# Performance work log

Hardware: AMD Instinct MI355X
Metric: run time of the kernel (lower is better)

## Reference

```python
import jax, jax.numpy as jnp
import numpy as np

N_KERNELS = 11

def _kernel_mus(n):
    l = [1.0]
    bs = 2.0 / (n - 1)
    l.append(1 - bs / 2)
    for i in range(1, n - 1):
        l.append(l[i] - bs)
    return l

def _kernel_sigmas(n):
    bs = 2.0 / (n - 1)
    return [0.001] + [0.5 * bs] * (n - 1)

MU = jnp.asarray(_kernel_mus(N_KERNELS), jnp.float32)      # [K]
SIGMA = jnp.asarray(_kernel_sigmas(N_KERNELS), jnp.float32)  # [K]


def setup_inputs() -> dict:
    key = jax.random.key(0)
    ks = jax.random.split(key, 10)
    V, E, C = 50000, 300, 128
    B, Q, D = 128, 30, 200
    inp = {
        'query_tokens': jax.random.randint(ks[0], (B, Q), 0, V),
        'document_tokens': jax.random.randint(ks[1], (B, D), 0, V),
        'embedding': jax.random.normal(ks[2], (V, E), jnp.float32) * 0.1,
        'conv_w1': jax.random.normal(ks[3], (C, E, 1), jnp.float32) * 0.05,
        'conv_w2': jax.random.normal(ks[4], (C, E, 2), jnp.float32) * 0.05,
        'conv_w3': jax.random.normal(ks[5], (C, E, 3), jnp.float32) * 0.05,
        'conv_b1': jax.random.normal(ks[6], (C,), jnp.float32) * 0.01,
        'conv_b2': jax.random.normal(ks[7], (C,), jnp.float32) * 0.01,
        'conv_b3': jax.random.normal(ks[8], (C,), jnp.float32) * 0.01,
        'dense_w': jax.random.uniform(ks[9], (1, N_KERNELS * 9), jnp.float32, -0.014, 0.014),
    }
    return inp


def _conv_ngram(x_ble, w, b):
    # x_ble: [B, L, E]; w: [C, E, k]; pad (0, k-1) on the length dim -> same length out
    x = x_ble.transpose(0, 2, 1)  # [B, E, L]
    y = jax.lax.conv_general_dilated(
        x, w, window_strides=(1,), padding=[(0, w.shape[2] - 1)],
        dimension_numbers=('NCH', 'OIH', 'NCH'))
    return jax.nn.relu(y + b[None, :, None]).transpose(0, 2, 1)  # [B, L, C]


def _kernel_pool(q, d, qd_mask, q_mask):
    # q: [B,Q,C], d: [B,D,C]; cosine sim -> Gaussian RBF soft-binning -> masked log-sum pooling
    qn = q / (jnp.linalg.norm(q, axis=-1, keepdims=True) + 1e-13)
    dn = d / (jnp.linalg.norm(d, axis=-1, keepdims=True) + 1e-13)
    cos = jnp.einsum('bqc,bdc->bqd', qn, dn) * qd_mask           # [B,Q,D]
    diff = cos[..., None] - MU                                    # [B,Q,D,K]
    kern = jnp.exp(-(diff * diff) / (2.0 * SIGMA * SIGMA)) * qd_mask[..., None]
    per_kernel_query = jnp.sum(kern, axis=2)                      # [B,Q,K]
    logk = jnp.log(jnp.clip(per_kernel_query, 1e-10)) * 0.01
    return jnp.sum(logk * q_mask[..., None], axis=1)              # [B,K]


def reference(query_tokens, document_tokens, embedding,
              conv_w1, conv_w2, conv_w3, conv_b1, conv_b2, conv_b3, dense_w):
    q_mask = (query_tokens > 0).astype(jnp.float32)               # [B,Q]
    d_mask = (document_tokens > 0).astype(jnp.float32)            # [B,D]
    qd_mask = q_mask[:, :, None] * d_mask[:, None, :]             # [B,Q,D]

    q_emb = embedding[query_tokens]                               # [B,Q,E]
    d_emb = embedding[document_tokens]                            # [B,D,E]

    convs = [(conv_w1, conv_b1), (conv_w2, conv_b2), (conv_w3, conv_b3)]
    q_grams = [_conv_ngram(q_emb, w, b) for w, b in convs]
    d_grams = [_conv_ngram(d_emb, w, b) for w, b in convs]

    feats = jnp.concatenate(
        [_kernel_pool(q, d, qd_mask, q_mask) for q in q_grams for d in d_grams],
        axis=1)                                                   # [B, K*9]
    return (feats @ dense_w.T)[:, 0]                              # [B]
```

## Files before the change

### kernel.cpp

```cpp
#include <hip/hip_runtime.h>
#include <hip/hip_bf16.h>
#include <math.h>

#define B_   128
#define Qn   30
#define Dn   200
#define En   300

typedef __attribute__((ext_vector_type(8))) short short8;
typedef __attribute__((ext_vector_type(4))) float floatx4;
typedef unsigned int u32;
typedef unsigned short u16;

typedef const __attribute__((address_space(1))) unsigned int* gas_ptr;
typedef __attribute__((address_space(3))) unsigned int* las_ptr;

static __device__ __forceinline__ void gld_lds16(const void* g, void* l) {
    __builtin_amdgcn_global_load_lds((gas_ptr)g, (las_ptr)l, 16, 0, 0);
}

static __device__ __forceinline__ u16 f2b(float x) {
    union { float f; u32 u; } v; v.f = x;
    u32 r = v.u + 0x7FFFu + ((v.u >> 16) & 1u);
    return (u16)(r >> 16);
}
static __device__ __forceinline__ float bits2f(u32 u) {
    union { u32 u2; float f; } v; v.u2 = u; return v.f;
}

__global__ void prep_gather_kernel(
    const int* __restrict__ qtok, const int* __restrict__ dtok,
    const float* __restrict__ emb,
    const float* __restrict__ w1, const float* __restrict__ w2, const float* __restrict__ w3,
    u16* __restrict__ Ag, u16* __restrict__ Wt2)
{
    const int tid = threadIdx.x;
    if (blockIdx.x < 16) {
        const int b = blockIdx.y, c = blockIdx.x;
        __shared__ int toks[16];
        if (tid < 16) {
            int pos = c*16 + tid;
            int tok = -1;
            if (pos < Dn) tok = dtok[b*Dn + pos];
            else if (pos >= 208 && pos < 238) tok = qtok[b*Qn + (pos - 208)];
            toks[tid] = tok;
        }
        __syncthreads();
        #pragma unroll
        for (int i = 0; i < 5; ++i) {
            int f = tid + i*256;
            int r = f / 80, c4 = f - r*80;
            int t = toks[r];
            u16 o0=0,o1=0,o2=0,o3=0;
            if (t >= 0 && c4 < 75) {
                float4 v = *(const float4*)(emb + t*En + c4*4);
                o0=f2b(v.x); o1=f2b(v.y); o2=f2b(v.z); o3=f2b(v.w);
            }
            u16* p = Ag + ((b*256 + c*16 + r)*320 + c4*4);
            p[0]=o0; p[1]=o1; p[2]=o2; p[3]=o3;
        }
        if (b == 127 && c == 15 && tid < 160) {
            u16* p = Ag + (32768*320) + tid*4;
            p[0]=0; p[1]=0; p[2]=0; p[3]=0;
        }
    } else {
        int p = ((blockIdx.x - 16)*128 + blockIdx.y)*256 + tid;
        if (p >= 245760) return;
        int g, ntap, o;
        if (p < 40960)       { g=0; ntap=1; o=p; }
        else if (p < 122880) { g=1; ntap=2; o=p-40960; }
        else                 { g=2; ntap=3; o=p-122880; }
        int ks = o / (ntap*4096);
        int r  = o - ks*(ntap*4096);
        int j  = r / 4096;
        int r2 = r & 4095;
        int nt = r2 >> 9;
        int r3 = r2 & 511;
        int q4 = r3 >> 7;
        int c16 = (r3 >> 3) & 15;
        int k8 = r3 & 7;
        int ch = nt*16 + c16;
        int e  = ks*32 + q4*8 + k8;
        float v = 0.f;
        if (e < En) {
            if (g == 0)      v = w1[ch*En + e];
            else if (g == 1) v = w2[(ch*En + e)*2 + j];
            else             v = w3[(ch*En + e)*3 + j];
        }
        Wt2[p] = f2b(v);
    }
}

template<int NTAP>
static __device__ __forceinline__ void conv_body(
    const u16* __restrict__ Ag, const u16* __restrict__ Wt2g,
    const float* __restrict__ bp,
    u16* __restrict__ qg, u16* __restrict__ dg,
    float* __restrict__ invnq, float* __restrict__ invnd,
    int gram, char* smem)
{
    char* As = smem;
    char* Bs = smem + 43296;

    const int tid = threadIdx.x;
    const int tile = blockIdx.x;
    const int wv = tid >> 6, lane = tid & 63;
    const int l15 = lane & 15, qd4 = lane >> 4;
    const int mh = wv >> 1, nh = wv & 1;

    {
        const char* src = (const char*)Wt2g + lane*16;
        #pragma unroll
        for (int i = 0; i < NTAP*2; ++i) {
            int chunk = wv*NTAP*2 + i;
            gld_lds16(src + chunk*1024, Bs + chunk*1024);
        }
    }
    {
        const char* base = (const char*)Ag + (size_t)tile*64*640;
        #pragma unroll
        for (int i = 0; i < 11; ++i) {
            int idx = tid + i*256;
            if (idx < 2640) {
                int r = idx / 40, c = idx - r*40;
                uint4 v = *(const uint4*)(base + r*640 + c*16);
                *(uint4*)(As + r*656 + c*16) = v;
            }
        }
    }

    float bias[4];
    #pragma unroll
    for (int nt = 0; nt < 4; ++nt) bias[nt] = bp[nh*64 + nt*16 + l15];

    floatx4 acc[2][4];
    #pragma unroll
    for (int mt = 0; mt < 2; ++mt)
        #pragma unroll
        for (int nt = 0; nt < 4; ++nt)
            acc[mt][nt] = (floatx4){0.f,0.f,0.f,0.f};

    __syncthreads();

    short8 af[2][NTAP];
    #pragma unroll
    for (int mt = 0; mt < 2; ++mt)
        #pragma unroll
        for (int j = 0; j < NTAP; ++j)
            af[mt][j] = *(const short8*)(As + (mh*32 + mt*16 + l15 + j)*656 + qd4*16);

    for (int ks = 0; ks < 10; ++ks) {
        #pragma unroll
        for (int j = 0; j < NTAP; ++j) {
            short8 bfj[4];
            #pragma unroll
            for (int nt = 0; nt < 4; ++nt)
                bfj[nt] = *(const short8*)(Bs + (j*8 + nh*4 + nt)*1024 + lane*16);
            #pragma unroll
            for (int mt = 0; mt < 2; ++mt)
                #pragma unroll
                for (int nt = 0; nt < 4; ++nt)
                    acc[mt][nt] = __builtin_amdgcn_mfma_f32_16x16x32_bf16(
                        af[mt][j], bfj[nt], acc[mt][nt], 0, 0, 0);
        }
        if (ks < 9) {
            __syncthreads();
            const char* src = (const char*)Wt2g + (ks+1)*NTAP*8192 + lane*16;
            #pragma unroll
            for (int i = 0; i < NTAP*2; ++i) {
                int chunk = wv*NTAP*2 + i;
                gld_lds16(src + chunk*1024, Bs + chunk*1024);
            }
            #pragma unroll
            for (int mt = 0; mt < 2; ++mt)
                #pragma unroll
                for (int j = 0; j < NTAP; ++j)
                    af[mt][j] = *(const short8*)(As + (mh*32 + mt*16 + l15 + j)*656 + (ks+1)*64 + qd4*16);
            __syncthreads();
        }
    }
    __syncthreads();

    u16* Gs = (u16*)Bs;
    #pragma unroll
    for (int mt = 0; mt < 2; ++mt)
        #pragma unroll
        for (int nt = 0; nt < 4; ++nt) {
            int ch = nh*64 + nt*16 + l15;
            #pragma unroll
            for (int i = 0; i < 4; ++i) {
                int row = mh*32 + mt*16 + qd4*4 + i;
                Gs[row*136 + ch] = f2b(fmaxf(acc[mt][nt][i] + bias[nt], 0.f));
            }
        }
    __syncthreads();

    if (tid < 64) {
        const char* rp = (const char*)Gs + tid*272;
        float ssum = 0.f;
        #pragma unroll
        for (int t16 = 0; t16 < 16; ++t16) {
            uint4 u = *(const uint4*)(rp + t16*16);
            float x;
            x = bits2f(u.x << 16); ssum += x*x;  x = bits2f(u.x & 0xffff0000u); ssum += x*x;
            x = bits2f(u.y << 16); ssum += x*x;  x = bits2f(u.y & 0xffff0000u); ssum += x*x;
            x = bits2f(u.z << 16); ssum += x*x;  x = bits2f(u.z & 0xffff0000u); ssum += x*x;
            x = bits2f(u.w << 16); ssum += x*x;  x = bits2f(u.w & 0xffff0000u); ssum += x*x;
        }
        float inv = 1.f / (sqrtf(ssum) + 1e-13f);
        int gR = tile*64 + tid;
        int b = gR >> 8, pos = gR & 255;
        if (pos < 208)                     invnd[(gram*B_ + b)*208 + pos] = inv;
        else if (pos < 240)                invnq[(gram*B_ + b)*32 + (pos - 208)] = inv;
    }
    #pragma unroll
    for (int i = 0; i < 4; ++i) {
        int idx = tid + i*256;
        int r = idx >> 4, c16 = idx & 15;
        uint4 v = *(const uint4*)((const char*)Gs + r*272 + c16*16);
        int gR = tile*64 + r;
        int b = gR >> 8, pos = gR & 255;
        if (pos < 208)      *(uint4*)(dg + ((gram*B_ + b)*208 + pos)*128 + c16*8) = v;
        else if (pos < 240) *(uint4*)(qg + ((gram*B_ + b)*32 + (pos - 208))*128 + c16*8) = v;
    }
}

__global__ __launch_bounds__(256, 2) void conv_kernel(
    const u16* __restrict__ Ag, const u16* __restrict__ Wt2,
    const float* __restrict__ b1, const float* __restrict__ b2, const float* __restrict__ b3,
    u16* __restrict__ qg, u16* __restrict__ dg,
    float* __restrict__ invnq, float* __restrict__ invnd)
{
    extern __shared__ char smem[];
    if (blockIdx.y == 0)
        conv_body<1>(Ag, Wt2,                       b1, qg, dg, invnq, invnd, 0, smem);
    else if (blockIdx.y == 1)
        conv_body<2>(Ag, Wt2 + 40960,               b2, qg, dg, invnq, invnd, 1, smem);
    else
        conv_body<3>(Ag, Wt2 + 122880,              b3, qg, dg, invnq, invnd, 2, smem);
}

__global__ __launch_bounds__(256, 2) void pool_kernel(
    const u16* __restrict__ qg, const u16* __restrict__ dg,
    const float* __restrict__ invnq, const float* __restrict__ invnd,
    const int* __restrict__ qtok, const int* __restrict__ dtok,
    float* __restrict__ feats)
{
    __shared__ __align__(16) u16 dsb[208*136];
    __shared__ float pk[32*12];
    __shared__ float invq[32];
    __shared__ float qm[32];
    __shared__ __align__(16) float invd[208];

    const int tid = threadIdx.x;
    const int b = blockIdx.y, combo = blockIdx.x;
    const int qi = combo / 3, dj = combo - 3*qi;
    const int wv = tid >> 6, lane = tid & 63;
    const int l15 = lane & 15, qd4 = lane >> 4;

    for (int idx = tid; idx < 208*16; idx += 256) {
        int r = idx >> 4, ch = idx & 15;
        uint4 v = make_uint4(0u,0u,0u,0u);
        if (r < Dn) v = *(const uint4*)(dg + ((dj*B_ + b)*208 + r)*128 + ch*8);
        *(uint4*)((char*)dsb + r*272 + ch*16) = v;
    }
    if (tid < 208) {
        float v = invnd[(dj*B_ + b)*208 + tid];
        bool ok = (tid < Dn) && (dtok[b*Dn + tid] > 0);
        invd[tid] = ok ? v : (-fabsf(v) - 1.0f);
    }
    if (tid < 32) {
        float v = invnq[(qi*B_ + b)*32 + tid];
        bool ok = (tid < Qn) && (qtok[b*Qn + tid] > 0);
        invq[tid] = ok ? v : 0.f;
        qm[tid] = ok ? 1.f : 0.f;
    }
    for (int i = tid; i < 384; i += 256) pk[i] = 0.f;
    __syncthreads();

    short8 qf[2][4];
    float vq[2];
    #pragma unroll
    for (int qt = 0; qt < 2; ++qt) {
        vq[qt] = invq[qt*16 + l15];
        #pragma unroll
        for (int ks = 0; ks < 4; ++ks)
            qf[qt][ks] = *(const short8*)(qg + ((qi*B_ + b)*32 + qt*16 + l15)*128 + ks*32 + qd4*8);
    }
    float pkl[2][11];
    #pragma unroll
    for (int qt = 0; qt < 2; ++qt)
        #pragma unroll
        for (int k = 0; k < 11; ++k) pkl[qt][k] = 0.f;

    const float CkR[9] = {8886110.5f, 162754.79f, 2980.958f, 54.598150f, 1.0f,
                          0.018315639f, 3.3546263e-4f, 6.1442124e-6f, 1.1253517e-7f};

    for (int t = wv; t < 13; t += 4) {
        short8 af[4];
        #pragma unroll
        for (int ks = 0; ks < 4; ++ks)
            af[ks] = *(const short8*)((const char*)dsb + (t*16 + l15)*272 + ks*64 + qd4*16);
        floatx4 acc[2];
        acc[0] = (floatx4){0.f,0.f,0.f,0.f};
        acc[1] = (floatx4){0.f,0.f,0.f,0.f};
        #pragma unroll
        for (int ks = 0; ks < 4; ++ks)
            #pragma unroll
            for (int qt = 0; qt < 2; ++qt)
                acc[qt] = __builtin_amdgcn_mfma_f32_16x16x32_bf16(af[ks], qf[qt][ks], acc[qt], 0, 0, 0);
        floatx4 iv4 = *(const floatx4*)(invd + t*16 + qd4*4);
        #pragma unroll
        for (int qt = 0; qt < 2; ++qt)
            #pragma unroll
            for (int i = 0; i < 4; ++i) {
                float cs = acc[qt][i] * vq[qt] * iv4[i];
                cs = (cs > 0.f) ? cs : 2.0f;
                float t0 = cs - 1.0f;
                float u  = cs - 0.9f;
                float s0 = __expf(-500000.f * t0 * t0);
                float e  = __expf(-50.f * u * u);
                float rr = __expf(-20.f * cs);
                pkl[qt][0] += s0;
                pkl[qt][1] += e;
                #pragma unroll
                for (int kk = 0; kk < 9; ++kk) {
                    e = e * rr * CkR[kk];
                    pkl[qt][2 + kk] += e;
                }
            }
    }
    #pragma unroll
    for (int qt = 0; qt < 2; ++qt)
        #pragma unroll
        for (int k = 0; k < 11; ++k) {
            float v = pkl[qt][k];
            v += __shfl_xor(v, 16);
            v += __shfl_xor(v, 32);
            if (qd4 == 0) atomicAdd(&pk[(qt*16 + l15)*12 + k], v);
        }
    __syncthreads();

    if (tid < 11) {
        float s = 0.f;
        for (int q = 0; q < Qn; ++q)
            s += qm[q] * 0.01f * __logf(fmaxf(pk[q*12 + tid], 1e-10f));
        feats[(b*9 + combo)*11 + tid] = s;
    }
}

__global__ void final_kernel(const float* __restrict__ feats,
                             const float* __restrict__ dw,
                             float* __restrict__ out) {
    int b = threadIdx.x;
    if (b < B_) {
        float s = 0.f;
        for (int f = 0; f < 99; ++f) s += feats[b*99 + f] * dw[f];
        out[b] = s;
    }
}

extern "C" void kernel_launch(void* const* d_in, const int* in_sizes, int n_in,
                              void* d_out, int out_size, void* d_ws, size_t ws_size,
                              hipStream_t stream) {
    const int*   qtok = (const int*)d_in[0];
    const int*   dtok = (const int*)d_in[1];
    const float* emb  = (const float*)d_in[2];
    const float* w1   = (const float*)d_in[3];
    const float* w2   = (const float*)d_in[4];
    const float* w3   = (const float*)d_in[5];
    const float* b1   = (const float*)d_in[6];
    const float* b2   = (const float*)d_in[7];
    const float* b3   = (const float*)d_in[8];
    const float* dw   = (const float*)d_in[9];
    float* out = (float*)d_out;

    char* w = (char*)d_ws;
    u16*   Wt2   = (u16*)w;
    u16*   Ag    = (u16*)(w + 491520);
    u16*   qg    = (u16*)(w + 21464320);
    u16*   dgm   = (u16*)(w + 24610048);
    float* invq_ = (float*)(w + 45057280);
    float* invd_ = (float*)(w + 45106432);
    float* feats = (float*)(w + 45425920);

    prep_gather_kernel<<<dim3(24, B_), 256, 0, stream>>>(
        qtok, dtok, emb, w1, w2, w3, Ag, Wt2);

    const int conv_lds = 43296 + 24576;
    hipFuncSetAttribute(reinterpret_cast<const void*>(conv_kernel),
                        hipFuncAttributeMaxDynamicSharedMemorySize, conv_lds);
    conv_kernel<<<dim3(512, 3), 256, conv_lds, stream>>>(
        Ag, Wt2, b1, b2, b3, qg, dgm, invq_, invd_);

    pool_kernel<<<dim3(9, B_), 256, 0, stream>>>(qg, dgm, invq_, invd_, qtok, dtok, feats);

    final_kernel<<<1, 128, 0, stream>>>(feats, dw, out);
}
```

Before: 194.5 us.

## Fuse embedding gather into conv, double-buffer weights, split trigram tiles, share doc tiles in pool

```diff
diff --git a/kernel.cpp b/kernel.cpp
--- a/kernel.cpp
+++ b/kernel.cpp
@@ -28,105 +28,87 @@
     union { u32 u2; float f; } v; v.u2 = u; return v.f;
 }
 
-__global__ void prep_gather_kernel(
+__global__ void prep_w_kernel(const float* __restrict__ w1, const float* __restrict__ w2,
+                              const float* __restrict__ w3, u16* __restrict__ Wt2) {
+    int p = blockIdx.x * 256 + threadIdx.x;
+    if (p >= 245760) return;
+    int g, ntap, o;
+    if (p < 40960)       { g=0; ntap=1; o=p; }
+    else if (p < 122880) { g=1; ntap=2; o=p-40960; }
+    else                 { g=2; ntap=3; o=p-122880; }
+    int ks = o / (ntap*4096);
+    int r  = o - ks*(ntap*4096);
+    int j  = r / 4096;
+    int r2 = r & 4095;
+    int nt = r2 >> 9;
+    int r3 = r2 & 511;
+    int q4 = r3 >> 7;
+    int c16 = (r3 >> 3) & 15;
+    int k8 = r3 & 7;
+    int ch = nt*16 + c16;
+    int e  = ks*32 + q4*8 + k8;
+    float v = 0.f;
+    if (e < En) {
+        if (g == 0)      v = w1[ch*En + e];
+        else if (g == 1) v = w2[(ch*En + e)*2 + j];
+        else             v = w3[(ch*En + e)*3 + j];
+    }
+    Wt2[p] = f2b(v);
+}
+
+template<int NTAP>
+static __device__ __forceinline__ void conv_body64(
+    int tile, int gram,
     const int* __restrict__ qtok, const int* __restrict__ dtok,
-    const float* __restrict__ emb,
-    const float* __restrict__ w1, const float* __restrict__ w2, const float* __restrict__ w3,
-    u16* __restrict__ Ag, u16* __restrict__ Wt2)
-{
-    const int tid = threadIdx.x;
-    if (blockIdx.x < 16) {
-        const int b = blockIdx.y, c = blockIdx.x;
-        __shared__ int toks[16];
-        if (tid < 16) {
-            int pos = c*16 + tid;
-            int tok = -1;
-            if (pos < Dn) tok = dtok[b*Dn + pos];
-            else if (pos >= 208 && pos < 238) tok = qtok[b*Qn + (pos - 208)];
-            toks[tid] = tok;
-        }
-        __syncthreads();
-        #pragma unroll
-        for (int i = 0; i < 5; ++i) {
-            int f = tid + i*256;
-            int r = f / 80, c4 = f - r*80;
-            int t = toks[r];
-            u16 o0=0,o1=0,o2=0,o3=0;
-            if (t >= 0 && c4 < 75) {
-                float4 v = *(const float4*)(emb + t*En + c4*4);
-                o0=f2b(v.x); o1=f2b(v.y); o2=f2b(v.z); o3=f2b(v.w);
-            }
-            u16* p = Ag + ((b*256 + c*16 + r)*320 + c4*4);
-            p[0]=o0; p[1]=o1; p[2]=o2; p[3]=o3;
-        }
-        if (b == 127 && c == 15 && tid < 160) {
-            u16* p = Ag + (32768*320) + tid*4;
-            p[0]=0; p[1]=0; p[2]=0; p[3]=0;
-        }
-    } else {
-        int p = ((blockIdx.x - 16)*128 + blockIdx.y)*256 + tid;
-        if (p >= 245760) return;
-        int g, ntap, o;
-        if (p < 40960)       { g=0; ntap=1; o=p; }
-        else if (p < 122880) { g=1; ntap=2; o=p-40960; }
-        else                 { g=2; ntap=3; o=p-122880; }
-        int ks = o / (ntap*4096);
-        int r  = o - ks*(ntap*4096);
-        int j  = r / 4096;
-        int r2 = r & 4095;
-        int nt = r2 >> 9;
-        int r3 = r2 & 511;
-        int q4 = r3 >> 7;
-        int c16 = (r3 >> 3) & 15;
-        int k8 = r3 & 7;
-        int ch = nt*16 + c16;
-        int e  = ks*32 + q4*8 + k8;
-        float v = 0.f;
-        if (e < En) {
-            if (g == 0)      v = w1[ch*En + e];
-            else if (g == 1) v = w2[(ch*En + e)*2 + j];
-            else             v = w3[(ch*En + e)*3 + j];
-        }
-        Wt2[p] = f2b(v);
-    }
-}
-
-template<int NTAP>
-static __device__ __forceinline__ void conv_body(
-    const u16* __restrict__ Ag, const u16* __restrict__ Wt2g,
+    const float* __restrict__ emb, const u16* __restrict__ Wt2g,
     const float* __restrict__ bp,
     u16* __restrict__ qg, u16* __restrict__ dg,
-    float* __restrict__ invnq, float* __restrict__ invnd,
-    int gram, char* smem)
+    float* __restrict__ invnq, float* __restrict__ invnd, char* smem)
 {
-    char* As = smem;
-    char* Bs = smem + 43296;
+    char* As  = smem;
+    char* Bs0 = smem + 43296;
+    char* Bs1 = smem + 43296 + NTAP*8192;
+    __shared__ int toks[66];
 
     const int tid = threadIdx.x;
-    const int tile = blockIdx.x;
     const int wv = tid >> 6, lane = tid & 63;
     const int l15 = lane & 15, qd4 = lane >> 4;
     const int mh = wv >> 1, nh = wv & 1;
 
+    if (tid < 66) {
+        int gR = tile*64 + tid;
+        int tok = -1;
+        if (gR < 32768) {
+            int bb = gR >> 8, pos = gR & 255;
+            if (pos < Dn) tok = dtok[bb*Dn + pos];
+            else if (pos >= 208 && pos < 238) tok = qtok[bb*Qn + (pos - 208)];
+        }
+        toks[tid] = tok;
+    }
+    __syncthreads();
+
     {
         const char* src = (const char*)Wt2g + lane*16;
         #pragma unroll
         for (int i = 0; i < NTAP*2; ++i) {
             int chunk = wv*NTAP*2 + i;
-            gld_lds16(src + chunk*1024, Bs + chunk*1024);
-        }
-    }
-    {
-        const char* base = (const char*)Ag + (size_t)tile*64*640;
-        #pragma unroll
-        for (int i = 0; i < 11; ++i) {
-            int idx = tid + i*256;
-            if (idx < 2640) {
-                int r = idx / 40, c = idx - r*40;
-                uint4 v = *(const uint4*)(base + r*640 + c*16);
-                *(uint4*)(As + r*656 + c*16) = v;
-            }
-        }
+            gld_lds16(src + chunk*1024, Bs0 + chunk*1024);
+        }
+    }
+    for (int f = tid; f < 66*75; f += 256) {
+        int row = f / 75, e4 = f - row*75;
+        int t = toks[row];
+        u16 o0=0,o1=0,o2=0,o3=0;
+        if (t >= 0) {
+            float4 v = *(const float4*)(emb + t*En + e4*4);
+            o0=f2b(v.x); o1=f2b(v.y); o2=f2b(v.z); o3=f2b(v.w);
+        }
+        u16* pp = (u16*)(As + row*656 + e4*8);
+        pp[0]=o0; pp[1]=o1; pp[2]=o2; pp[3]=o3;
+    }
+    for (int f = tid; f < 66*14; f += 256) {
+        int row = f / 14, cc = f - row*14;
+        *(u32*)(As + row*656 + 600 + cc*4) = 0u;
     }
 
     float bias[4];
@@ -142,20 +124,29 @@
 
     __syncthreads();
 
-    short8 af[2][NTAP];
-    #pragma unroll
-    for (int mt = 0; mt < 2; ++mt)
-        #pragma unroll
-        for (int j = 0; j < NTAP; ++j)
-            af[mt][j] = *(const short8*)(As + (mh*32 + mt*16 + l15 + j)*656 + qd4*16);
-
     for (int ks = 0; ks < 10; ++ks) {
+        char* Bcur = (ks & 1) ? Bs1 : Bs0;
+        char* Bnxt = (ks & 1) ? Bs0 : Bs1;
+        if (ks < 9) {
+            const char* src = (const char*)Wt2g + (ks+1)*NTAP*8192 + lane*16;
+            #pragma unroll
+            for (int i = 0; i < NTAP*2; ++i) {
+                int chunk = wv*NTAP*2 + i;
+                gld_lds16(src + chunk*1024, Bnxt + chunk*1024);
+            }
+        }
+        short8 af[2][NTAP];
+        #pragma unroll
+        for (int mt = 0; mt < 2; ++mt)
+            #pragma unroll
+            for (int j = 0; j < NTAP; ++j)
+                af[mt][j] = *(const short8*)(As + (mh*32 + mt*16 + l15 + j)*656 + ks*64 + qd4*16);
         #pragma unroll
         for (int j = 0; j < NTAP; ++j) {
             short8 bfj[4];
             #pragma unroll
             for (int nt = 0; nt < 4; ++nt)
-                bfj[nt] = *(const short8*)(Bs + (j*8 + nh*4 + nt)*1024 + lane*16);
+                bfj[nt] = *(const short8*)(Bcur + (j*8 + nh*4 + nt)*1024 + lane*16);
             #pragma unroll
             for (int mt = 0; mt < 2; ++mt)
                 #pragma unroll
@@ -163,25 +154,10 @@
                     acc[mt][nt] = __builtin_amdgcn_mfma_f32_16x16x32_bf16(
                         af[mt][j], bfj[nt], acc[mt][nt], 0, 0, 0);
         }
-        if (ks < 9) {
-            __syncthreads();
-            const char* src = (const char*)Wt2g + (ks+1)*NTAP*8192 + lane*16;
-            #pragma unroll
-            for (int i = 0; i < NTAP*2; ++i) {
-                int chunk = wv*NTAP*2 + i;
-                gld_lds16(src + chunk*1024, Bs + chunk*1024);
-            }
-            #pragma unroll
-            for (int mt = 0; mt < 2; ++mt)
-                #pragma unroll
-                for (int j = 0; j < NTAP; ++j)
-                    af[mt][j] = *(const short8*)(As + (mh*32 + mt*16 + l15 + j)*656 + (ks+1)*64 + qd4*16);
-            __syncthreads();
-        }
-    }
-    __syncthreads();
-
-    u16* Gs = (u16*)Bs;
+        __syncthreads();
+    }
+
+    u16* Gs = (u16*)As;
     #pragma unroll
     for (int mt = 0; mt < 2; ++mt)
         #pragma unroll
@@ -210,8 +186,8 @@
         float inv = 1.f / (sqrtf(ssum) + 1e-13f);
         int gR = tile*64 + tid;
         int b = gR >> 8, pos = gR & 255;
-        if (pos < 208)                     invnd[(gram*B_ + b)*208 + pos] = inv;
-        else if (pos < 240)                invnq[(gram*B_ + b)*32 + (pos - 208)] = inv;
+        if (pos < 208)      invnd[(gram*B_ + b)*208 + pos] = inv;
+        else if (pos < 238) invnq[(gram*B_ + b)*32 + (pos - 208)] = inv;
     }
     #pragma unroll
     for (int i = 0; i < 4; ++i) {
@@ -221,23 +197,168 @@
         int gR = tile*64 + r;
         int b = gR >> 8, pos = gR & 255;
         if (pos < 208)      *(uint4*)(dg + ((gram*B_ + b)*208 + pos)*128 + c16*8) = v;
-        else if (pos < 240) *(uint4*)(qg + ((gram*B_ + b)*32 + (pos - 208))*128 + c16*8) = v;
+        else if (pos < 238) *(uint4*)(qg + ((gram*B_ + b)*32 + (pos - 208))*128 + c16*8) = v;
+    }
+}
+
+static __device__ __forceinline__ void conv_body32(
+    int tile,
+    const int* __restrict__ qtok, const int* __restrict__ dtok,
+    const float* __restrict__ emb, const u16* __restrict__ Wt2g,
+    const float* __restrict__ bp,
+    u16* __restrict__ qg, u16* __restrict__ dg,
+    float* __restrict__ invnq, float* __restrict__ invnd, char* smem)
+{
+    char* As  = smem;
+    char* Bs0 = smem + 22304;
+    char* Bs1 = smem + 46880;
+    __shared__ int toks[34];
+
+    const int tid = threadIdx.x;
+    const int wv = tid >> 6, lane = tid & 63;
+    const int l15 = lane & 15, qd4 = lane >> 4;
+
+    if (tid < 34) {
+        int gR = tile*32 + tid;
+        int tok = -1;
+        if (gR < 32768) {
+            int bb = gR >> 8, pos = gR & 255;
+            if (pos < Dn) tok = dtok[bb*Dn + pos];
+            else if (pos >= 208 && pos < 238) tok = qtok[bb*Qn + (pos - 208)];
+        }
+        toks[tid] = tok;
+    }
+    __syncthreads();
+
+    {
+        const char* src = (const char*)Wt2g + lane*16;
+        #pragma unroll
+        for (int i = 0; i < 6; ++i) {
+            int chunk = wv*6 + i;
+            gld_lds16(src + chunk*1024, Bs0 + chunk*1024);
+        }
+    }
+    for (int f = tid; f < 34*75; f += 256) {
+        int row = f / 75, e4 = f - row*75;
+        int t = toks[row];
+        u16 o0=0,o1=0,o2=0,o3=0;
+        if (t >= 0) {
+            float4 v = *(const float4*)(emb + t*En + e4*4);
+            o0=f2b(v.x); o1=f2b(v.y); o2=f2b(v.z); o3=f2b(v.w);
+        }
+        u16* pp = (u16*)(As + row*656 + e4*8);
+        pp[0]=o0; pp[1]=o1; pp[2]=o2; pp[3]=o3;
+    }
+    for (int f = tid; f < 34*14; f += 256) {
+        int row = f / 14, cc = f - row*14;
+        *(u32*)(As + row*656 + 600 + cc*4) = 0u;
+    }
+
+    float bias[2];
+    #pragma unroll
+    for (int nt = 0; nt < 2; ++nt) bias[nt] = bp[wv*32 + nt*16 + l15];
+
+    floatx4 acc[2][2];
+    #pragma unroll
+    for (int mt = 0; mt < 2; ++mt)
+        #pragma unroll
+        for (int nt = 0; nt < 2; ++nt)
+            acc[mt][nt] = (floatx4){0.f,0.f,0.f,0.f};
+
+    __syncthreads();
+
+    for (int ks = 0; ks < 10; ++ks) {
+        char* Bcur = (ks & 1) ? Bs1 : Bs0;
+        char* Bnxt = (ks & 1) ? Bs0 : Bs1;
+        if (ks < 9) {
+            const char* src = (const char*)Wt2g + (ks+1)*24576 + lane*16;
+            #pragma unroll
+            for (int i = 0; i < 6; ++i) {
+                int chunk = wv*6 + i;
+                gld_lds16(src + chunk*1024, Bnxt + chunk*1024);
+            }
+        }
+        short8 af[2][3];
+        #pragma unroll
+        for (int mt = 0; mt < 2; ++mt)
+            #pragma unroll
+            for (int j = 0; j < 3; ++j)
+                af[mt][j] = *(const short8*)(As + (mt*16 + l15 + j)*656 + ks*64 + qd4*16);
+        #pragma unroll
+        for (int j = 0; j < 3; ++j) {
+            short8 bfj[2];
+            #pragma unroll
+            for (int nt = 0; nt < 2; ++nt)
+                bfj[nt] = *(const short8*)(Bcur + (j*8 + wv*2 + nt)*1024 + lane*16);
+            #pragma unroll
+            for (int mt = 0; mt < 2; ++mt)
+                #pragma unroll
+                for (int nt = 0; nt < 2; ++nt)
+                    acc[mt][nt] = __builtin_amdgcn_mfma_f32_16x16x32_bf16(
+                        af[mt][j], bfj[nt], acc[mt][nt], 0, 0, 0);
+        }
+        __syncthreads();
+    }
+
+    u16* Gs = (u16*)As;
+    #pragma unroll
+    for (int mt = 0; mt < 2; ++mt)
+        #pragma unroll
+        for (int nt = 0; nt < 2; ++nt) {
+            int ch = wv*32 + nt*16 + l15;
+            #pragma unroll
+            for (int i = 0; i < 4; ++i) {
+                int row = mt*16 + qd4*4 + i;
+                Gs[row*136 + ch] = f2b(fmaxf(acc[mt][nt][i] + bias[nt], 0.f));
+            }
+        }
+    __syncthreads();
+
+    if (tid < 32) {
+        const char* rp = (const char*)Gs + tid*272;
+        float ssum = 0.f;
+        #pragma unroll
+        for (int t16 = 0; t16 < 16; ++t16) {
+            uint4 u = *(const uint4*)(rp + t16*16);
+            float x;
+            x = bits2f(u.x << 16); ssum += x*x;  x = bits2f(u.x & 0xffff0000u); ssum += x*x;
+            x = bits2f(u.y << 16); ssum += x*x;  x = bits2f(u.y & 0xffff0000u); ssum += x*x;
+            x = bits2f(u.z << 16); ssum += x*x;  x = bits2f(u.z & 0xffff0000u); ssum += x*x;
+            x = bits2f(u.w << 16); ssum += x*x;  x = bits2f(u.w & 0xffff0000u); ssum += x*x;
+        }
+        float inv = 1.f / (sqrtf(ssum) + 1e-13f);
+        int gR = tile*32 + tid;
+        int b = gR >> 8, pos = gR & 255;
+        if (pos < 208)      invnd[(2*B_ + b)*208 + pos] = inv;
+        else if (pos < 238) invnq[(2*B_ + b)*32 + (pos - 208)] = inv;
+    }
+    #pragma unroll
+    for (int i = 0; i < 2; ++i) {
+        int idx = tid + i*256;
+        int r = idx >> 4, c16 = idx & 15;
+        uint4 v = *(const uint4*)((const char*)Gs + r*272 + c16*16);
+        int gR = tile*32 + r;
+        int b = gR >> 8, pos = gR & 255;
+        if (pos < 208)      *(uint4*)(dg + ((2*B_ + b)*208 + pos)*128 + c16*8) = v;
+        else if (pos < 238) *(uint4*)(qg + ((2*B_ + b)*32 + (pos - 208))*128 + c16*8) = v;
     }
 }
 
 __global__ __launch_bounds__(256, 2) void conv_kernel(
-    const u16* __restrict__ Ag, const u16* __restrict__ Wt2,
+    const int* __restrict__ qtok, const int* __restrict__ dtok,
+    const float* __restrict__ emb, const u16* __restrict__ Wt2,
     const float* __restrict__ b1, const float* __restrict__ b2, const float* __restrict__ b3,
     u16* __restrict__ qg, u16* __restrict__ dg,
     float* __restrict__ invnq, float* __restrict__ invnd)
 {
     extern __shared__ char smem[];
-    if (blockIdx.y == 0)
-        conv_body<1>(Ag, Wt2,                       b1, qg, dg, invnq, invnd, 0, smem);
-    else if (blockIdx.y == 1)
-        conv_body<2>(Ag, Wt2 + 40960,               b2, qg, dg, invnq, invnd, 1, smem);
+    int bx = blockIdx.x;
+    if (bx < 512)
+        conv_body64<1>(bx, 0, qtok, dtok, emb, Wt2,          b1, qg, dg, invnq, invnd, smem);
+    else if (bx < 1024)
+        conv_body64<2>(bx-512, 1, qtok, dtok, emb, Wt2+40960, b2, qg, dg, invnq, invnd, smem);
     else
-        conv_body<3>(Ag, Wt2 + 122880,              b3, qg, dg, invnq, invnd, 2, smem);
+        conv_body32(bx-1024, qtok, dtok, emb, Wt2+122880,     b3, qg, dg, invnq, invnd, smem);
 }
 
 __global__ __launch_bounds__(256, 2) void pool_kernel(
@@ -247,14 +368,13 @@
     float* __restrict__ feats)
 {
     __shared__ __align__(16) u16 dsb[208*136];
-    __shared__ float pk[32*12];
-    __shared__ float invq[32];
-    __shared__ float qm[32];
+    __shared__ float pk[96*12];
+    __shared__ float invqA[96];
+    __shared__ float qmA[96];
     __shared__ __align__(16) float invd[208];
 
     const int tid = threadIdx.x;
-    const int b = blockIdx.y, combo = blockIdx.x;
-    const int qi = combo / 3, dj = combo - 3*qi;
+    const int b = blockIdx.y, dj = blockIdx.x;
     const int wv = tid >> 6, lane = tid & 63;
     const int l15 = lane & 15, qd4 = lane >> 4;
 
@@ -269,83 +389,87 @@
         bool ok = (tid < Dn) && (dtok[b*Dn + tid] > 0);
         invd[tid] = ok ? v : (-fabsf(v) - 1.0f);
     }
-    if (tid < 32) {
-        float v = invnq[(qi*B_ + b)*32 + tid];
-        bool ok = (tid < Qn) && (qtok[b*Qn + tid] > 0);
-        invq[tid] = ok ? v : 0.f;
-        qm[tid] = ok ? 1.f : 0.f;
-    }
-    for (int i = tid; i < 384; i += 256) pk[i] = 0.f;
-    __syncthreads();
-
-    short8 qf[2][4];
-    float vq[2];
-    #pragma unroll
-    for (int qt = 0; qt < 2; ++qt) {
-        vq[qt] = invq[qt*16 + l15];
-        #pragma unroll
-        for (int ks = 0; ks < 4; ++ks)
-            qf[qt][ks] = *(const short8*)(qg + ((qi*B_ + b)*32 + qt*16 + l15)*128 + ks*32 + qd4*8);
-    }
-    float pkl[2][11];
-    #pragma unroll
-    for (int qt = 0; qt < 2; ++qt)
-        #pragma unroll
-        for (int k = 0; k < 11; ++k) pkl[qt][k] = 0.f;
+    if (tid < 96) {
+        int qi = tid >> 5, qr = tid & 31;
+        float v = invnq[(qi*B_ + b)*32 + qr];
+        bool ok = (qr < Qn) && (qtok[b*Qn + qr] > 0);
+        invqA[tid] = ok ? v : 0.f;
+        qmA[tid] = ok ? 1.f : 0.f;
+    }
+    for (int i = tid; i < 96*12; i += 256) pk[i] = 0.f;
+    __syncthreads();
 
     const float CkR[9] = {8886110.5f, 162754.79f, 2980.958f, 54.598150f, 1.0f,
                           0.018315639f, 3.3546263e-4f, 6.1442124e-6f, 1.1253517e-7f};
 
-    for (int t = wv; t < 13; t += 4) {
-        short8 af[4];
-        #pragma unroll
-        for (int ks = 0; ks < 4; ++ks)
-            af[ks] = *(const short8*)((const char*)dsb + (t*16 + l15)*272 + ks*64 + qd4*16);
-        floatx4 acc[2];
-        acc[0] = (floatx4){0.f,0.f,0.f,0.f};
-        acc[1] = (floatx4){0.f,0.f,0.f,0.f};
-        #pragma unroll
-        for (int ks = 0; ks < 4; ++ks)
+    for (int qi = 0; qi < 3; ++qi) {
+        short8 qf[2][4];
+        float vq[2];
+        #pragma unroll
+        for (int qt = 0; qt < 2; ++qt) {
+            vq[qt] = invqA[qi*32 + qt*16 + l15];
+            #pragma unroll
+            for (int ks = 0; ks < 4; ++ks)
+                qf[qt][ks] = *(const short8*)(qg + ((qi*B_ + b)*32 + qt*16 + l15)*128 + ks*32 + qd4*8);
+        }
+        float pkl[2][11];
+        #pragma unroll
+        for (int qt = 0; qt < 2; ++qt)
+            #pragma unroll
+            for (int k = 0; k < 11; ++k) pkl[qt][k] = 0.f;
+
+        for (int t = wv; t < 13; t += 4) {
+            short8 af[4];
+            #pragma unroll
+            for (int ks = 0; ks < 4; ++ks)
+                af[ks] = *(const short8*)((const char*)dsb + (t*16 + l15)*272 + ks*64 + qd4*16);
+            floatx4 acc[2];
+            acc[0] = (floatx4){0.f,0.f,0.f,0.f};
+            acc[1] = (floatx4){0.f,0.f,0.f,0.f};
+            #pragma unroll
+            for (int ks = 0; ks < 4; ++ks)
+                #pragma unroll
+                for (int qt = 0; qt < 2; ++qt)
+                    acc[qt] = __builtin_amdgcn_mfma_f32_16x16x32_bf16(af[ks], qf[qt][ks], acc[qt], 0, 0, 0);
+            floatx4 iv4 = *(const floatx4*)(invd + t*16 + qd4*4);
             #pragma unroll
             for (int qt = 0; qt < 2; ++qt)
-                acc[qt] = __builtin_amdgcn_mfma_f32_16x16x32_bf16(af[ks], qf[qt][ks], acc[qt], 0, 0, 0);
-        floatx4 iv4 = *(const floatx4*)(invd + t*16 + qd4*4);
+                #pragma unroll
+                for (int i = 0; i < 4; ++i) {
+                    float cs = acc[qt][i] * vq[qt] * iv4[i];
+                    cs = (cs > 0.f) ? cs : 2.0f;
+                    float t0 = cs - 1.0f;
+                    float u  = cs - 0.9f;
+                    float s0 = __expf(-500000.f * t0 * t0);
+                    float e  = __expf(-50.f * u * u);
+                    float rr = __expf(-20.f * cs);
+                    pkl[qt][0] += s0;
+                    pkl[qt][1] += e;
+                    #pragma unroll
+                    for (int kk = 0; kk < 9; ++kk) {
+                        e = e * rr * CkR[kk];
+                        pkl[qt][2 + kk] += e;
+                    }
+                }
+        }
         #pragma unroll
         for (int qt = 0; qt < 2; ++qt)
             #pragma unroll
-            for (int i = 0; i < 4; ++i) {
-                float cs = acc[qt][i] * vq[qt] * iv4[i];
-                cs = (cs > 0.f) ? cs : 2.0f;
-                float t0 = cs - 1.0f;
-                float u  = cs - 0.9f;
-                float s0 = __expf(-500000.f * t0 * t0);
-                float e  = __expf(-50.f * u * u);
-                float rr = __expf(-20.f * cs);
-                pkl[qt][0] += s0;
-                pkl[qt][1] += e;
-                #pragma unroll
-                for (int kk = 0; kk < 9; ++kk) {
-                    e = e * rr * CkR[kk];
-                    pkl[qt][2 + kk] += e;
-                }
+            for (int k = 0; k < 11; ++k) {
+                float v = pkl[qt][k];
+                v += __shfl_xor(v, 16);
+                v += __shfl_xor(v, 32);
+                if (qd4 == 0) atomicAdd(&pk[(qi*32 + qt*16 + l15)*12 + k], v);
             }
     }
-    #pragma unroll
-    for (int qt = 0; qt < 2; ++qt)
-        #pragma unroll
-        for (int k = 0; k < 11; ++k) {
-            float v = pkl[qt][k];
-            v += __shfl_xor(v, 16);
-            v += __shfl_xor(v, 32);
-            if (qd4 == 0) atomicAdd(&pk[(qt*16 + l15)*12 + k], v);
-        }
-    __syncthreads();
-
-    if (tid < 11) {
+    __syncthreads();
+
+    if (tid < 33) {
+        int qi = tid / 11, k = tid - qi*11;
         float s = 0.f;
         for (int q = 0; q < Qn; ++q)
-            s += qm[q] * 0.01f * __logf(fmaxf(pk[q*12 + tid], 1e-10f));
-        feats[(b*9 + combo)*11 + tid] = s;
+            s += qmA[qi*32 + q] * 0.01f * __logf(fmaxf(pk[(qi*32 + q)*12 + k], 1e-10f));
+        feats[(b*9 + qi*3 + dj)*11 + k] = s;
     }
 }
 
@@ -377,23 +501,21 @@
 
     char* w = (char*)d_ws;
     u16*   Wt2   = (u16*)w;
-    u16*   Ag    = (u16*)(w + 491520);
-    u16*   qg    = (u16*)(w + 21464320);
-    u16*   dgm   = (u16*)(w + 24610048);
-    float* invq_ = (float*)(w + 45057280);
-    float* invd_ = (float*)(w + 45106432);
-    float* feats = (float*)(w + 45425920);
-
-    prep_gather_kernel<<<dim3(24, B_), 256, 0, stream>>>(
-        qtok, dtok, emb, w1, w2, w3, Ag, Wt2);
-
-    const int conv_lds = 43296 + 24576;
+    u16*   qg    = (u16*)(w + 491520);
+    u16*   dgm   = (u16*)(w + 3637248);
+    float* invq_ = (float*)(w + 24084480);
+    float* invd_ = (float*)(w + 24133632);
+    float* feats = (float*)(w + 24453120);
+
+    prep_w_kernel<<<960, 256, 0, stream>>>(w1, w2, w3, Wt2);
+
+    const int conv_lds = 76064;
     hipFuncSetAttribute(reinterpret_cast<const void*>(conv_kernel),
                         hipFuncAttributeMaxDynamicSharedMemorySize, conv_lds);
-    conv_kernel<<<dim3(512, 3), 256, conv_lds, stream>>>(
-        Ag, Wt2, b1, b2, b3, qg, dgm, invq_, invd_);
-
-    pool_kernel<<<dim3(9, B_), 256, 0, stream>>>(qg, dgm, invq_, invd_, qtok, dtok, feats);
+    conv_kernel<<<dim3(2048), 256, conv_lds, stream>>>(
+        qtok, dtok, emb, Wt2, b1, b2, b3, qg, dgm, invq_, invd_);
+
+    pool_kernel<<<dim3(3, B_), 256, 0, stream>>>(qg, dgm, invq_, invd_, qtok, dtok, feats);
 
     final_kernel<<<1, 128, 0, stream>>>(feats, dw, out);
 }
```

Measured after the change: 269.1 us. +38.3%, slower.
